# Kernel optimization log

Hardware: AMD Instinct MI355X
Metric: run time of the kernel (lower is better)

The kernel has to match this reference:

```python
import jax, jax.numpy as jnp
import numpy as np

N = 10000   # nodes (cells)
E = 100000  # edges
G = 2000    # num_genes
H = 20      # heads
C1 = 128    # layer-1 out channels per head
C2 = 128    # latent_dim
NEG_SLOPE = 0.2


def setup_inputs():
    key = jax.random.key(0)
    ks = jax.random.split(key, 9)
    s = 0.05
    return {
        "x": jax.random.normal(ks[0], (N, G), jnp.float32),
        "edge_index": jax.random.randint(ks[1], (2, E), 0, N, dtype=jnp.int64),
        "W1": jax.random.normal(ks[2], (G, H * C1), jnp.float32) * s,
        "att_src1": jax.random.normal(ks[3], (H, C1), jnp.float32) * s,
        "att_dst1": jax.random.normal(ks[4], (H, C1), jnp.float32) * s,
        "b1": jnp.zeros((H * C1,), jnp.float32),
        "W2": jax.random.normal(ks[5], (H * C1, H * C2), jnp.float32) * s,
        "att_src2": jax.random.normal(ks[6], (H, C2), jnp.float32) * s,
        "att_dst2": jax.random.normal(ks[7], (H, C2), jnp.float32) * s,
        "b2": jnp.zeros((C2,), jnp.float32),
    }


def _gat_conv(x, W, att_src, att_dst, bias, src, dst, concat):
    """PyG GATConv (eval mode, self-loops already in src/dst)."""
    n = x.shape[0]
    h_, c_ = att_src.shape
    h = (x @ W).reshape(n, h_, c_)                      # [N, H, C]
    a_src = jnp.einsum("nhc,hc->nh", h, att_src)        # [N, H]
    a_dst = jnp.einsum("nhc,hc->nh", h, att_dst)        # [N, H]
    e = a_src[src] + a_dst[dst]                          # [E, H]
    e = jnp.where(e > 0, e, NEG_SLOPE * e)               # leaky_relu
    # segment softmax over incoming edges of each destination node
    e_max = jax.ops.segment_max(e, dst, num_segments=n)  # [N, H]
    ex = jnp.exp(e - e_max[dst])                         # [E, H]
    denom = jax.ops.segment_sum(ex, dst, num_segments=n)
    alpha = ex / denom[dst]                              # [E, H]
    msg = alpha[:, :, None] * h[src]                     # [E, H, C]
    out = jax.ops.segment_sum(msg, dst, num_segments=n)  # [N, H, C]
    if concat:
        out = out.reshape(n, h_ * c_)
    else:
        out = out.mean(axis=1)                           # [N, C]
    return out + bias


def reference(x, edge_index, W1, att_src1, att_dst1, b1, W2, att_src2, att_dst2, b2):
    n = x.shape[0]
    loop = jnp.arange(n, dtype=edge_index.dtype)
    src = jnp.concatenate([edge_index[0], loop])  # PyG add_self_loops=True
    dst = jnp.concatenate([edge_index[1], loop])
    h1 = _gat_conv(x, W1, att_src1, att_dst1, b1, src, dst, concat=True)
    h1 = jax.nn.relu(h1)  # dropout is identity in eval mode
    h2 = _gat_conv(h1, W2, att_src2, att_dst2, b2, src, dst, concat=False)
    return jax.nn.relu(h2)
```

## Files before the change

### kernel.cpp

```cpp
#include <hip/hip_runtime.h>

#define NEG_SLOPE 0.2f

typedef __attribute__((ext_vector_type(4))) float floatx4;
typedef __attribute__((ext_vector_type(8))) short shortx8;

__device__ __forceinline__ unsigned short f2bf(float f) {
  union { float f; unsigned int u; } v;
  v.f = f;
  unsigned int r = (v.u + 0x7FFFu + ((v.u >> 16) & 1u)) >> 16;
  return (unsigned short)r;
}
__device__ __forceinline__ float bf2f(unsigned short u) {
  union { unsigned int u; float f; } v;
  v.u = (unsigned int)u << 16;
  return v.f;
}
__device__ __forceinline__ void store_out(float* p, float v) { *p = v; }
__device__ __forceinline__ void store_out(unsigned short* p, float v) { *p = f2bf(v); }

__device__ __forceinline__ void gload_lds16(const unsigned short* g, unsigned short* l) {
  __builtin_amdgcn_global_load_lds(
      (const __attribute__((address_space(1))) void*)(g),
      (__attribute__((address_space(3))) void*)(l), 16, 0, 0);
}

__device__ __forceinline__ int load_edge(const void* ei, long idx, int is64) {
  if (is64) return (int)((const long long*)ei)[idx];
  return ((const int*)ei)[idx];
}

__global__ void detect64_kernel(const unsigned int* __restrict__ p, int* __restrict__ flag) {
  int is64 = 1;
  for (int i = 0; i < 32; ++i)
    if (p[2 * i + 1] != 0u) is64 = 0;
  *flag = is64;
}

__global__ void init_cnt_kernel(int* __restrict__ cnt, int n) {
  int i = blockIdx.x * blockDim.x + threadIdx.x;
  if (i < n) cnt[i] = 1;
}

__global__ void count_kernel(const void* __restrict__ ei, const int* __restrict__ flag, int E,
                             int* __restrict__ cnt) {
  int e = blockIdx.x * blockDim.x + threadIdx.x;
  if (e >= E) return;
  int is64 = *flag;
  int d = load_edge(ei, (long)E + e, is64);
  atomicAdd(&cnt[d], 1);
}

__global__ __launch_bounds__(1024) void scan_kernel(const int* __restrict__ cnt,
                                                    int* __restrict__ offs, int n) {
  __shared__ int partial[1024];
  int t = threadIdx.x;
  int per = (n + 1023) / 1024;
  int beg = t * per;
  int end = min(beg + per, n);
  int sum = 0;
  for (int i = beg; i < end; ++i) sum += cnt[i];
  partial[t] = sum;
  __syncthreads();
  for (int d = 1; d < 1024; d <<= 1) {
    int v = (t >= d) ? partial[t - d] : 0;
    __syncthreads();
    partial[t] += v;
    __syncthreads();
  }
  int excl = (t == 0) ? 0 : partial[t - 1];
  for (int i = beg; i < end; ++i) { offs[i] = excl; excl += cnt[i]; }
  if (t == 1023) offs[n] = partial[1023];
}

__global__ void init_self_kernel(const int* __restrict__ offs, int* __restrict__ srcs,
                                 int* __restrict__ fill, int n) {
  int i = blockIdx.x * blockDim.x + threadIdx.x;
  if (i < n) { srcs[offs[i]] = i; fill[i] = 1; }
}

__global__ void scatter_kernel(const void* __restrict__ ei, const int* __restrict__ flag, int E,
                               const int* __restrict__ offs, int* __restrict__ fill,
                               int* __restrict__ srcs) {
  int e = blockIdx.x * blockDim.x + threadIdx.x;
  if (e >= E) return;
  int is64 = *flag;
  int s = load_edge(ei, e, is64);
  int d = load_edge(ei, (long)E + e, is64);
  int pos = offs[d] + atomicAdd(&fill[d], 1);
  srcs[pos] = s;
}


__global__ __launch_bounds__(256) void pack_a_kernel(const float* __restrict__ in,
                                                     unsigned short* __restrict__ out, int M,
                                                     int K, int Kpad) {
  int rt = blockIdx.x;
  int r = threadIdx.x & 127;
  int kq = threadIdx.x >> 7;
  int row = rt * 128 + r;
  int nkc = Kpad >> 3;
  unsigned short* obase = out + (long)rt * Kpad * 128 + r * 8;
  const float* irow = in + (long)row * K;
  for (int kc = kq + (int)blockIdx.y * 2; kc < nkc; kc += (int)gridDim.y * 2) {
    int k = kc << 3;
    shortx8 o;
    if (row < M && k + 8 <= K && (K & 3) == 0) {
      float4 v0 = *(const float4*)(irow + k);
      float4 v1 = *(const float4*)(irow + k + 4);
      o[0] = (short)f2bf(v0.x); o[1] = (short)f2bf(v0.y);
      o[2] = (short)f2bf(v0.z); o[3] = (short)f2bf(v0.w);
      o[4] = (short)f2bf(v1.x); o[5] = (short)f2bf(v1.y);
      o[6] = (short)f2bf(v1.z); o[7] = (short)f2bf(v1.w);
    } else {
#pragma unroll
      for (int i = 0; i < 8; ++i) {
        int kk = k + i;
        float v = (row < M && kk < K) ? irow[kk] : 0.f;
        o[i] = (short)f2bf(v);
      }
    }
    *(shortx8*)(obase + (long)kc * 1024) = o;
  }
}

__global__ __launch_bounds__(256) void transpose_pack_kernel(const float* __restrict__ in,
                                                             unsigned short* __restrict__ out,
                                                             int K, int N, int Kpad) {
  __shared__ float tile[32][33];
  int kb = blockIdx.x * 32;
  int nb = blockIdx.y * 32;
  int tx = threadIdx.x & 31;
  int ty = threadIdx.x >> 5;
#pragma unroll
  for (int i = 0; i < 32; i += 8) {
    int k = kb + ty + i;
    tile[ty + i][tx] = (k < K) ? in[(long)k * N + nb + tx] : 0.f;
  }
  __syncthreads();
  if (threadIdx.x < 128) {
    int nl = threadIdx.x & 31;
    int nn = nb + nl;
    int kc4 = threadIdx.x >> 5;
    int k0 = kc4 * 8;
    shortx8 o;
#pragma unroll
    for (int j = 0; j < 8; ++j) o[j] = (short)f2bf(tile[k0 + j][nl]);
    int kc = (kb >> 3) + kc4;
    *(shortx8*)(out + (long)(nn >> 7) * Kpad * 128 + (long)kc * 1024 + (nn & 127) * 8) = o;
  }
}

template <typename OT, int AMODE>
__global__ __launch_bounds__(256) void mfma_gemm_kernel(const unsigned short* __restrict__ A,
                                                        const unsigned short* __restrict__ Bt,
                                                        OT* __restrict__ C, int M, int N, int K) {
  __shared__ unsigned short As[2][4096];
  __shared__ unsigned short Bs[2][4096];

  int tid = threadIdx.x;
  int lane = tid & 63;
  int w = tid >> 6;
  int wm = w & 1, wn = w >> 1;
  int bn = blockIdx.x * 128;
  int bm = blockIdx.y * 128;
  int quad = lane >> 4, l16 = lane & 15;

  int row = tid & 127;
  int p = tid >> 7;

  const unsigned short* pA;
  unsigned short* laA;
  long aStep;
  int aOff2;
  if (AMODE == 0) {
    pA = A + (long)(bm >> 7) * K * 128 + tid * 8;
    laA = &As[0][0] + w * 512;
    aStep = 4096;
    aOff2 = 2048;
  } else {
    pA = A + (long)(bm + row) * K + p * 8;
    laA = &As[0][0] + (w >> 1) * 1024 + (w & 1) * 512;
    aStep = 32;
    aOff2 = 16;
  }
  const unsigned short* pB = Bt + (long)(bn >> 7) * K * 128 + tid * 8;
  unsigned short* lb = &Bs[0][0] + w * 512;

  floatx4 acc[4][4];
#pragma unroll
  for (int i = 0; i < 4; ++i)
#pragma unroll
    for (int j = 0; j < 4; ++j) acc[i][j] = (floatx4){0.f, 0.f, 0.f, 0.f};

  gload_lds16(pA, laA);
  gload_lds16(pA + aOff2, laA + 2048);
  gload_lds16(pB, lb);
  gload_lds16(pB + 2048, lb + 2048);

  int nk = K >> 5;
  for (int k = 0; k < nk; ++k) {
    int cur = k & 1;
    if (k + 1 < nk) {
      const unsigned short* qA = pA + (long)(k + 1) * aStep;
      const unsigned short* qB = pB + (long)(k + 1) * 4096;
      unsigned short* da = laA + (cur ^ 1) * 4096;
      unsigned short* db = lb + (cur ^ 1) * 4096;
      gload_lds16(qA, da);
      gload_lds16(qA + aOff2, da + 2048);
      gload_lds16(qB, db);
      gload_lds16(qB + 2048, db + 2048);
      __builtin_amdgcn_s_waitcnt(0x0F74);
    } else {
      __builtin_amdgcn_s_waitcnt(0x0F70);
    }
    __builtin_amdgcn_s_barrier();

    shortx8 a[4], b[4];
#pragma unroll
    for (int i = 0; i < 4; ++i) {
      a[i] = *(const shortx8*)(&As[cur][(quad * 128 + wm * 64 + i * 16 + l16) * 8]);
      b[i] = *(const shortx8*)(&Bs[cur][(quad * 128 + wn * 64 + i * 16 + l16) * 8]);
    }
#pragma unroll
    for (int i = 0; i < 4; ++i)
#pragma unroll
      for (int j = 0; j < 4; ++j)
        acc[i][j] = __builtin_amdgcn_mfma_f32_16x16x32_bf16(a[i], b[j], acc[i][j], 0, 0, 0);

    __builtin_amdgcn_s_barrier();
  }

  int orow0 = bm + wm * 64 + quad * 4;
  int ocol0 = bn + wn * 64 + l16;
#pragma unroll
  for (int i = 0; i < 4; ++i)
#pragma unroll
    for (int j = 0; j < 4; ++j)
#pragma unroll
      for (int r2 = 0; r2 < 4; ++r2) {
        int rr = orow0 + i * 16 + r2;
        if (rr < M) store_out(&C[(long)rr * N + ocol0 + j * 16], acc[i][j][r2]);
      }
}

__global__ __launch_bounds__(256) void att_coef_kernel(const unsigned short* __restrict__ h,
                                                       const float* __restrict__ att_s,
                                                       const float* __restrict__ att_d,
                                                       float* __restrict__ a_s,
                                                       float* __restrict__ a_d, int n, int H,
                                                       int C) {
  int wave = (int)((blockIdx.x * blockDim.x + threadIdx.x) >> 6);
  int lane = threadIdx.x & 63;
  if (wave >= n) return;
  const unsigned short* row = h + (long)wave * H * C;
  for (int hh = 0; hh < H; ++hh) {
    float s = 0.f, d = 0.f;
    for (int c = lane; c < C; c += 64) {
      float v = bf2f(row[hh * C + c]);
      s += v * att_s[hh * C + c];
      d += v * att_d[hh * C + c];
    }
#pragma unroll
    for (int o = 32; o > 0; o >>= 1) {
      s += __shfl_down(s, o, 64);
      d += __shfl_down(d, o, 64);
    }
    if (lane == 0) {
      a_s[(long)wave * H + hh] = s;
      a_d[(long)wave * H + hh] = d;
    }
  }
}

__global__ void edge_softmax_kernel(const float* __restrict__ a_src,
                                    const float* __restrict__ a_dst,
                                    const int* __restrict__ offs, const int* __restrict__ srcs,
                                    float* __restrict__ alpha, int n, int H) {
  int idx = blockIdx.x * blockDim.x + threadIdx.x;
  if (idx >= n * H) return;
  int dstn = idx / H;
  int hh = idx - dstn * H;
  int beg = offs[dstn], end = offs[dstn + 1];
  float ad = a_dst[idx];
  float m = -1e30f;
  for (int j = beg; j < end; ++j) {
    float e = a_src[srcs[j] * H + hh] + ad;
    e = e > 0.f ? e : NEG_SLOPE * e;
    m = fmaxf(m, e);
  }
  float ssum = 0.f;
  for (int j = beg; j < end; ++j) {
    float e = a_src[srcs[j] * H + hh] + ad;
    e = e > 0.f ? e : NEG_SLOPE * e;
    float ex = __expf(e - m);
    alpha[(long)j * H + hh] = ex;
    ssum += ex;
  }
  float inv = 1.f / ssum;
  for (int j = beg; j < end; ++j) alpha[(long)j * H + hh] *= inv;
}

__global__ __launch_bounds__(320) void aggregate1_kernel(const unsigned short* __restrict__ h,
                                                         const float* __restrict__ alpha,
                                                         const int* __restrict__ offs,
                                                         const int* __restrict__ srcs,
                                                         const float* __restrict__ bias,
                                                         unsigned short* __restrict__ out, int H,
                                                         int C, int HC) {
  int dstn = blockIdx.x;
  int t = threadIdx.x;
  int beg = offs[dstn], end = offs[dstn + 1];
  int nf8 = HC >> 3;
  for (int fid = t; fid < nf8; fid += blockDim.x) {
    int hh = (fid << 3) / C;
    float acc[8];
#pragma unroll
    for (int i = 0; i < 8; ++i) acc[i] = 0.f;
    for (int j = beg; j < end; ++j) {
      int s = srcs[j];
      float al = alpha[(long)j * H + hh];
      shortx8 r = ((const shortx8*)(h + (long)s * HC))[fid];
#pragma unroll
      for (int i = 0; i < 8; ++i) acc[i] = fmaf(al, bf2f((unsigned short)r[i]), acc[i]);
    }
    shortx8 o;
#pragma unroll
    for (int i = 0; i < 8; ++i) {
      float bb = bias[(fid << 3) + i];
      o[i] = (short)f2bf(fmaxf(acc[i] + bb, 0.f));
    }
    ((shortx8*)(out + (long)dstn * HC))[fid] = o;
  }
}

__global__ __launch_bounds__(128) void aggregate2_kernel(const unsigned short* __restrict__ h,
                                                         const float* __restrict__ alpha,
                                                         const int* __restrict__ offs,
                                                         const int* __restrict__ srcs,
                                                         const float* __restrict__ bias,
                                                         float* __restrict__ out, int H, int C) {
  int dstn = blockIdx.x;
  int c = threadIdx.x;
  if (c >= C) return;
  int beg = offs[dstn], end = offs[dstn + 1];
  int HC = H * C;
  float acc = 0.f;
  for (int j = beg; j < end; ++j) {
    int s = srcs[j];
    const unsigned short* row = h + (long)s * HC;
    const float* al = alpha + (long)j * H;
#pragma unroll 5
    for (int hh = 0; hh < H; ++hh) acc = fmaf(al[hh], bf2f(row[hh * C + c]), acc);
  }
  float v = acc * (1.f / (float)H) + bias[c];
  out[(long)dstn * C + c] = v > 0.f ? v : 0.f;
}

static inline size_t align256(size_t x) { return (x + 255) & ~(size_t)255; }

extern "C" void kernel_launch(void* const* d_in, const int* in_sizes, int n_in, void* d_out,
                              int out_size, void* d_ws, size_t ws_size, hipStream_t stream) {
  const float* x        = (const float*)d_in[0];
  const void*  ei       = d_in[1];
  const float* W1       = (const float*)d_in[2];
  const float* att_src1 = (const float*)d_in[3];
  const float* att_dst1 = (const float*)d_in[4];
  const float* b1       = (const float*)d_in[5];
  const float* W2       = (const float*)d_in[6];
  const float* att_src2 = (const float*)d_in[7];
  const float* att_dst2 = (const float*)d_in[8];
  const float* b2       = (const float*)d_in[9];
  float* out = (float*)d_out;

  const int C2  = in_sizes[9];
  const int H   = in_sizes[7] / C2;
  const int HC1 = in_sizes[5];
  const int C1  = HC1 / H;
  const int G   = in_sizes[2] / HC1;
  const int Nn  = in_sizes[0] / G;
  const int E   = in_sizes[1] / 2;
  const int HC2 = H * C2;
  const int Et  = E + Nn;
  const int Mpad = ((Nn + 127) / 128) * 128;
  const int K1pad = ((G + 31) / 32) * 32;

  char* p = (char*)d_ws;
  size_t off = 0;
  unsigned short* hb  = (unsigned short*)(p + off); off = align256(off + (size_t)Mpad * (HC1 > HC2 ? HC1 : HC2) * 2);
  unsigned short* xb  = (unsigned short*)(p + off); off = align256(off + (size_t)Mpad * K1pad * 2);
  unsigned short* xb2 = (unsigned short*)(p + off); off = align256(off + (size_t)Mpad * HC1 * 2);
  unsigned short* W1t = (unsigned short*)(p + off); off = align256(off + (size_t)HC1 * K1pad * 2);
  unsigned short* W2t = (unsigned short*)(p + off); off = align256(off + (size_t)HC2 * HC1 * 2);
  float* a_s   = (float*)(p + off); off = align256(off + (size_t)Nn * H * 4);
  float* a_d   = (float*)(p + off); off = align256(off + (size_t)Nn * H * 4);
  float* alpha = (float*)(p + off); off = align256(off + (size_t)Et * H * 4);
  int* cnt     = (int*)(p + off); off = align256(off + (size_t)Nn * 4);
  int* offs    = (int*)(p + off); off = align256(off + (size_t)(Nn + 1) * 4);
  int* fill    = (int*)(p + off); off = align256(off + (size_t)Nn * 4);
  int* srcs    = (int*)(p + off); off = align256(off + (size_t)Et * 4);
  int* flag64  = (int*)(p + off); off = align256(off + 16);
  (void)ws_size; (void)n_in; (void)out_size;

  const int TB = 256;
  detect64_kernel<<<1, 1, 0, stream>>>((const unsigned int*)ei, flag64);
  init_cnt_kernel<<<(Nn + TB - 1) / TB, TB, 0, stream>>>(cnt, Nn);
  count_kernel<<<(E + TB - 1) / TB, TB, 0, stream>>>(ei, flag64, E, cnt);
  scan_kernel<<<1, 1024, 0, stream>>>(cnt, offs, Nn);
  init_self_kernel<<<(Nn + TB - 1) / TB, TB, 0, stream>>>(offs, srcs, fill, Nn);
  scatter_kernel<<<(E + TB - 1) / TB, TB, 0, stream>>>(ei, flag64, E, offs, fill, srcs);

  {
    dim3 ga(Mpad / 128, 8);
    pack_a_kernel<<<ga, 256, 0, stream>>>(x, xb, Nn, G, K1pad);
    dim3 g1(K1pad / 32, HC1 / 32);
    transpose_pack_kernel<<<g1, 256, 0, stream>>>(W1, W1t, G, HC1, K1pad);
    dim3 g2(HC1 / 32, HC2 / 32);
    transpose_pack_kernel<<<g2, 256, 0, stream>>>(W2, W2t, HC1, HC2, HC1);
  }

  {
    dim3 grid(HC1 / 128, Mpad / 128);
    mfma_gemm_kernel<unsigned short, 0><<<grid, 256, 0, stream>>>(xb, W1t, hb, Nn, HC1, K1pad);
  }
  att_coef_kernel<<<(Nn + 3) / 4, 256, 0, stream>>>(hb, att_src1, att_dst1, a_s, a_d, Nn, H, C1);
  edge_softmax_kernel<<<(Nn * H + TB - 1) / TB, TB, 0, stream>>>(a_s, a_d, offs, srcs, alpha, Nn, H);
  aggregate1_kernel<<<Nn, 320, 0, stream>>>(hb, alpha, offs, srcs, b1, xb2, H, C1, HC1);

  {
    dim3 grid(HC2 / 128, Mpad / 128);
    mfma_gemm_kernel<unsigned short, 1><<<grid, 256, 0, stream>>>(xb2, W2t, hb, Nn, HC2, HC1);
  }
  att_coef_kernel<<<(Nn + 3) / 4, 256, 0, stream>>>(hb, att_src2, att_dst2, a_s, a_d, Nn, H, C2);
  edge_softmax_kernel<<<(Nn * H + TB - 1) / TB, TB, 0, stream>>>(a_s, a_d, offs, srcs, alpha, Nn, H);
  aggregate2_kernel<<<Nn, 128, 0, stream>>>(hb, alpha, offs, srcs, b2, out, H, C2);
}
```

Measured before the change: 904.2 us.

## Remap GEMM workgroups per XCD and widen layer-2 aggregation over heads

```diff
diff --git a/kernel.cpp b/kernel.cpp
--- a/kernel.cpp
+++ b/kernel.cpp
@@ -162,8 +162,16 @@
   int lane = tid & 63;
   int w = tid >> 6;
   int wm = w & 1, wn = w >> 1;
-  int bn = blockIdx.x * 128;
-  int bm = blockIdx.y * 128;
+
+  int nwg = (int)(gridDim.x * gridDim.y);
+  int orig = (int)(blockIdx.y * gridDim.x + blockIdx.x);
+  int q = nwg >> 3, r = nwg & 7;
+  int xcd = orig & 7;
+  int inx = orig >> 3;
+  int neu = (xcd < r ? xcd * (q + 1) : r * (q + 1) + (xcd - r) * q) + inx;
+  int bn = (neu % (int)gridDim.x) * 128;
+  int bm = (neu / (int)gridDim.x) * 128;
+
   int quad = lane >> 4, l16 = lane & 15;
 
   int row = tid & 127;
@@ -334,27 +342,42 @@
   }
 }
 
-__global__ __launch_bounds__(128) void aggregate2_kernel(const unsigned short* __restrict__ h,
+__global__ __launch_bounds__(320) void aggregate2_kernel(const unsigned short* __restrict__ h,
                                                          const float* __restrict__ alpha,
                                                          const int* __restrict__ offs,
                                                          const int* __restrict__ srcs,
                                                          const float* __restrict__ bias,
                                                          float* __restrict__ out, int H, int C) {
+  __shared__ float smem[256];
   int dstn = blockIdx.x;
-  int c = threadIdx.x;
-  if (c >= C) return;
+  int t = threadIdx.x;
+  int HC = H * C;
+  int nf8 = HC >> 3;
   int beg = offs[dstn], end = offs[dstn + 1];
-  int HC = H * C;
-  float acc = 0.f;
-  for (int j = beg; j < end; ++j) {
-    int s = srcs[j];
-    const unsigned short* row = h + (long)s * HC;
-    const float* al = alpha + (long)j * H;
-#pragma unroll 5
-    for (int hh = 0; hh < H; ++hh) acc = fmaf(al[hh], bf2f(row[hh * C + c]), acc);
-  }
-  float v = acc * (1.f / (float)H) + bias[c];
-  out[(long)dstn * C + c] = v > 0.f ? v : 0.f;
+  for (int c = t; c < C; c += blockDim.x) smem[c] = 0.f;
+  __syncthreads();
+  for (int fid = t; fid < nf8; fid += blockDim.x) {
+    int hh = (fid << 3) / C;
+    int c0 = (fid << 3) - hh * C;
+    float acc[8];
+#pragma unroll
+    for (int i = 0; i < 8; ++i) acc[i] = 0.f;
+    for (int j = beg; j < end; ++j) {
+      int s = srcs[j];
+      float al = alpha[(long)j * H + hh];
+      shortx8 r = ((const shortx8*)(h + (long)s * HC))[fid];
+#pragma unroll
+      for (int i = 0; i < 8; ++i) acc[i] = fmaf(al, bf2f((unsigned short)r[i]), acc[i]);
+    }
+#pragma unroll
+    for (int i = 0; i < 8; ++i) atomicAdd(&smem[c0 + i], acc[i]);
+  }
+  __syncthreads();
+  float invH = 1.f / (float)H;
+  for (int c = t; c < C; c += blockDim.x) {
+    float v = smem[c] * invH + bias[c];
+    out[(long)dstn * C + c] = v > 0.f ? v : 0.f;
+  }
 }
 
 static inline size_t align256(size_t x) { return (x + 255) & ~(size_t)255; }
@@ -433,5 +456,5 @@
   }
   att_coef_kernel<<<(Nn + 3) / 4, 256, 0, stream>>>(hb, att_src2, att_dst2, a_s, a_d, Nn, H, C2);
   edge_softmax_kernel<<<(Nn * H + TB - 1) / TB, TB, 0, stream>>>(a_s, a_d, offs, srcs, alpha, Nn, H);
-  aggregate2_kernel<<<Nn, 128, 0, stream>>>(hb, alpha, offs, srcs, b2, out, H, C2);
-}
+  aggregate2_kernel<<<Nn, 320, 0, stream>>>(hb, alpha, offs, srcs, b2, out, H, C2);
+}
```

Result: slower. 963.8 us (+6.6%).
